# Kernel optimization log

Hardware: AMD Instinct MI355X
Metric: run time of the kernel (lower is better)

The kernel has to match this reference:

```python
import jax, jax.numpy as jnp
import numpy as np

N, IN_F, OUT_F = 8192, 512, 64
ALPHA = 0.2  # LeakyReLU negative slope


def setup_inputs() -> dict:
    key = jax.random.key(0)
    k1, k2, k3, k4 = jax.random.split(key, 4)
    x = jax.random.normal(k1, (N, IN_F), dtype=jnp.float32)
    # dense 0/1 adjacency; Bernoulli(0.5) so every row has neighbors
    adj = jax.random.randint(k2, (N, N), 0, 2, dtype=jnp.int32)
    # W stored as [in, out] (torch Linear applies x @ W.T; equivalent math)
    W = jax.random.normal(k3, (IN_F, OUT_F), dtype=jnp.float32) / np.sqrt(IN_F)
    a = jax.random.normal(k4, (2 * OUT_F,), dtype=jnp.float32) * 0.1
    return {"x": x, "adj": adj, "W": W, "a": a}


def reference(x, adj, W, a):
    # Wh: [n, out]
    Wh = x @ W
    # concat([Wh_i, Wh_j]) @ a  ==  (Wh @ a1)_i + (Wh @ a2)_j  (split 'a' in halves)
    a1, a2 = a[:OUT_F], a[OUT_F:]
    e = (Wh @ a1)[:, None] + (Wh @ a2)[None, :]          # [n, n]
    e = jnp.where(e > 0, e, ALPHA * e)                    # LeakyReLU
    e = jnp.where(adj == 0, -jnp.inf, e)                  # mask non-edges
    attn = jax.nn.softmax(e, axis=1)                      # softmax over neighbors j
    # dropout omitted: eval mode (training=False)
    return attn @ Wh                                      # [n, out]
```

## Files before the change

kernel.cpp:

```cpp
#include <hip/hip_runtime.h>
#include <cstdint>
#include <cstddef>

#define NN 8192
#define INF 512
#define OUTF 64
#define ALPHA 0.2f
#define JSPLIT 512
#define NW32 (NN / 32)
#define GEMM_BLOCKS 512
#define RSTRIDE 36

typedef _Float16 half8 __attribute__((ext_vector_type(8)));
typedef float f32x4 __attribute__((ext_vector_type(4)));

static __device__ inline unsigned short f2h(float f) {
    _Float16 h = (_Float16)f;
    return __builtin_bit_cast(unsigned short, h);
}

__global__ __launch_bounds__(256) void k01_fused(
    const float* __restrict__ x, const int* __restrict__ adj,
    const float* __restrict__ W, const float* __restrict__ a,
    unsigned short* __restrict__ Asw, float* __restrict__ U,
    unsigned short* __restrict__ e2ph, unsigned short* __restrict__ e2nh,
    unsigned* __restrict__ mask)
{
    __shared__ int ldsbuf[8192];
    const int tid = threadIdx.x;

    if (blockIdx.x >= GEMM_BLOCKS) {
        const int row = blockIdx.x - GEMM_BLOCKS;
        const int* arow = adj + (size_t)row * NN;

        #pragma unroll
        for (int k = 0; k < 8; ++k) {
            const int i = k * 1024 + tid * 4;
            int4 v = *(const int4*)(arow + i);
            const int p = i ^ (((i >> 7) & 7) << 2);
            *(int4*)&ldsbuf[p] = v;
        }
        __syncthreads();

        unsigned m = 0;
        #pragma unroll
        for (int k = 0; k < 8; ++k) {
            const int i2 = tid * 32 + k * 4;
            const int p2 = i2 ^ (((i2 >> 7) & 7) << 2);
            int4 v = *(const int4*)&ldsbuf[p2];
            m |= (v.x != 0 ? 1u : 0u) << (4 * k);
            m |= (v.y != 0 ? 1u : 0u) << (4 * k + 1);
            m |= (v.z != 0 ? 1u : 0u) << (4 * k + 2);
            m |= (v.w != 0 ? 1u : 0u) << (4 * k + 3);
        }
        mask[(size_t)row * NW32 + tid] = m;
        return;
    }

    const int i0 = blockIdx.x * 16;
    const int w  = __builtin_amdgcn_readfirstlane(tid >> 6);
    const int c  = tid & 63;
    const float* xr = x + (size_t)(i0 + 4 * w) * INF;
    const float* Wc = W + c;
    float acc[4] = {0.f, 0.f, 0.f, 0.f};

    #pragma unroll 4
    for (int kk = 0; kk < 128; ++kk) {
        const float4 x0 = *(const float4*)(xr + 0 * INF + kk * 4);
        const float4 x1 = *(const float4*)(xr + 1 * INF + kk * 4);
        const float4 x2 = *(const float4*)(xr + 2 * INF + kk * 4);
        const float4 x3 = *(const float4*)(xr + 3 * INF + kk * 4);
        const float w0 = Wc[(kk * 4 + 0) * OUTF];
        const float w1 = Wc[(kk * 4 + 1) * OUTF];
        const float w2 = Wc[(kk * 4 + 2) * OUTF];
        const float w3 = Wc[(kk * 4 + 3) * OUTF];
        acc[0] = fmaf(x0.x, w0, fmaf(x0.y, w1, fmaf(x0.z, w2, fmaf(x0.w, w3, acc[0]))));
        acc[1] = fmaf(x1.x, w0, fmaf(x1.y, w1, fmaf(x1.z, w2, fmaf(x1.w, w3, acc[1]))));
        acc[2] = fmaf(x2.x, w0, fmaf(x2.y, w1, fmaf(x2.z, w2, fmaf(x2.w, w3, acc[2]))));
        acc[3] = fmaf(x3.x, w0, fmaf(x3.y, w1, fmaf(x3.z, w2, fmaf(x3.w, w3, acc[3]))));
    }

    const float a1c = a[c];
    const float a2c = a[64 + c];
    #pragma unroll
    for (int q = 0; q < 4; ++q) {
        float v1 = acc[q] * a1c;
        float v2 = acc[q] * a2c;
        #pragma unroll
        for (int m = 32; m; m >>= 1) {
            v1 += __shfl_xor(v1, m, 64);
            v2 += __shfl_xor(v2, m, 64);
        }
        if (c == 0) {
            const int i = i0 + 4 * w + q;
            U[i]    = __expf((1.0f - ALPHA) * v1);
            e2ph[i] = f2h(__expf(v2));
            e2nh[i] = f2h(__expf(ALPHA * v2));
        }
    }

    const int i   = i0 + 4 * w;
    const int jt  = i >> 5;
    const int sub = (i >> 3) & 3;
    const int e0  = i & 7;
    ushort4 pk;
    pk.x = f2h(acc[0]); pk.y = f2h(acc[1]);
    pk.z = f2h(acc[2]); pk.w = f2h(acc[3]);
    *(ushort4*)&Asw[((size_t)(c >> 4) * 256 + jt) * 512 + ((c & 15) + 16 * sub) * 8 + e0] = pk;
}

__global__ __launch_bounds__(1024, 4) void k2_final(
    const unsigned* __restrict__ mask, const unsigned short* __restrict__ Asw,
    const float* __restrict__ Ug, const unsigned short* __restrict__ e2ph,
    const unsigned short* __restrict__ e2nh,
    float* __restrict__ out)
{
    __shared__ float red[16 * 64 * RSTRIDE];
    __shared__ float redl[16 * 32];

    const int tid   = threadIdx.x;
    const int l     = tid & 63;
    const int w     = tid >> 6;
    const int i0    = blockIdx.x * 32;
    const int jbase = w * JSPLIT;
    const int jb32  = jbase >> 5;

    const int il  = l & 15;
    const int kg  = l >> 4;
    const int kg8 = kg * 8;

    const unsigned uaw = f2h(Ug[i0 + il]);
    const unsigned ubw = f2h(Ug[i0 + 16 + il]);
    const unsigned ua2 = uaw * 0x00010001u;
    const unsigned ub2 = ubw * 0x00010001u;

    const unsigned* mbase = mask + (size_t)(i0 + il) * NW32 + jb32 + kg;
    unsigned mA[4], mB[4];
    #pragma unroll
    for (int ss = 0; ss < 4; ++ss) {
        mA[ss] = mbase[ss * 4];
        mB[ss] = mbase[(size_t)16 * NW32 + ss * 4];
    }

    f32x4 a00 = {0,0,0,0}, a01 = {0,0,0,0}, a10 = {0,0,0,0}, a11 = {0,0,0,0};
    f32x4 a20 = {0,0,0,0}, a21 = {0,0,0,0}, a30 = {0,0,0,0}, a31 = {0,0,0,0};
    f32x4 sA  = {0,0,0,0}, sB  = {0,0,0,0};

    half8 ONESH;
    #pragma unroll
    for (int e = 0; e < 8; ++e) ONESH[e] = (_Float16)1.0f;

    uint4 epc = *(const uint4*)(e2ph + jbase + kg8);
    uint4 enc = *(const uint4*)(e2nh + jbase + kg8);
    unsigned bAc = (__shfl(mA[0], il, 64) >> kg8) & 0xffu;
    unsigned bBc = (__shfl(mB[0], il, 64) >> kg8) & 0xffu;

#define SPAIR(DST, U2, EPW, ENW, BITS, R) do {                                \
    unsigned mu_, mx_;                                                        \
    asm("v_pk_mul_f16 %0, %1, %2" : "=v"(mu_) : "v"(U2), "v"(EPW));           \
    asm("v_pk_max_f16 %0, %1, %2" : "=v"(mx_) : "v"(mu_), "v"(ENW));          \
    const int lo_ = (int)((BITS) << (31 - 2 * (R))) >> 31;                    \
    const int hi_ = (int)((BITS) << (30 - 2 * (R))) >> 31;                    \
    DST = mx_ & (((unsigned)hi_ & 0xFFFF0000u) | ((unsigned)lo_ & 0x0000FFFFu)); \
} while (0)

    #pragma unroll
    for (int t = 0; t < 16; ++t) {
        const unsigned short* Ac = Asw + (size_t)(jb32 + t) * 512 + l * 8;
        half8 A0c = *(const half8*)(Ac);
        half8 A1c = *(const half8*)(Ac + 131072);
        half8 A2c = *(const half8*)(Ac + 262144);
        half8 A3c = *(const half8*)(Ac + 393216);

        const int tn = (t < 15) ? t + 1 : t;
        uint4 epn = *(const uint4*)(e2ph + jbase + tn * 32 + kg8);
        uint4 enn = *(const uint4*)(e2nh + jbase + tn * 32 + kg8);
        const int ssn = tn >> 2, ksn = tn & 3;
        unsigned bAn = (__shfl(mA[ssn], il + 16 * ksn, 64) >> kg8) & 0xffu;
        unsigned bBn = (__shfl(mB[ssn], il + 16 * ksn, 64) >> kg8) & 0xffu;

        uint4 wa, wb;
        SPAIR(wa.x, ua2, epc.x, enc.x, bAc, 0);
        SPAIR(wa.y, ua2, epc.y, enc.y, bAc, 1);
        SPAIR(wa.z, ua2, epc.z, enc.z, bAc, 2);
        SPAIR(wa.w, ua2, epc.w, enc.w, bAc, 3);
        SPAIR(wb.x, ub2, epc.x, enc.x, bBc, 0);
        SPAIR(wb.y, ub2, epc.y, enc.y, bBc, 1);
        SPAIR(wb.z, ub2, epc.z, enc.z, bBc, 2);
        SPAIR(wb.w, ub2, epc.w, enc.w, bBc, 3);
        const half8 BA = __builtin_bit_cast(half8, wa);
        const half8 BB = __builtin_bit_cast(half8, wb);

        sA = __builtin_amdgcn_mfma_f32_16x16x32_f16(ONESH, BA, sA, 0, 0, 0);
        sB = __builtin_amdgcn_mfma_f32_16x16x32_f16(ONESH, BB, sB, 0, 0, 0);

        a00 = __builtin_amdgcn_mfma_f32_16x16x32_f16(A0c, BA, a00, 0, 0, 0);
        a01 = __builtin_amdgcn_mfma_f32_16x16x32_f16(A0c, BB, a01, 0, 0, 0);
        a10 = __builtin_amdgcn_mfma_f32_16x16x32_f16(A1c, BA, a10, 0, 0, 0);
        a11 = __builtin_amdgcn_mfma_f32_16x16x32_f16(A1c, BB, a11, 0, 0, 0);
        a20 = __builtin_amdgcn_mfma_f32_16x16x32_f16(A2c, BA, a20, 0, 0, 0);
        a21 = __builtin_amdgcn_mfma_f32_16x16x32_f16(A2c, BB, a21, 0, 0, 0);
        a30 = __builtin_amdgcn_mfma_f32_16x16x32_f16(A3c, BA, a30, 0, 0, 0);
        a31 = __builtin_amdgcn_mfma_f32_16x16x32_f16(A3c, BB, a31, 0, 0, 0);

        epc = epn; enc = enn;
        bAc = bAn; bBc = bBn;
    }
#undef SPAIR

    float* rw = red + (size_t)(w * 64 + l) * RSTRIDE;
    *(float4*)(rw + 0)  = *(float4*)&a00;
    *(float4*)(rw + 4)  = *(float4*)&a01;
    *(float4*)(rw + 8)  = *(float4*)&a10;
    *(float4*)(rw + 12) = *(float4*)&a11;
    *(float4*)(rw + 16) = *(float4*)&a20;
    *(float4*)(rw + 20) = *(float4*)&a21;
    *(float4*)(rw + 24) = *(float4*)&a30;
    *(float4*)(rw + 28) = *(float4*)&a31;
    if (l < 16) {
        redl[w * 32 + il]      = sA[0];
        redl[w * 32 + 16 + il] = sB[0];
    }
    __syncthreads();

    const int row = tid >> 5;
    const int n0  = (tid & 31) * 2;
    const int h   = row >> 4;
    const int il2 = row & 15;

    float den = 0.f;
    #pragma unroll
    for (int w2 = 0; w2 < 16; ++w2) den += redl[w2 * 32 + row];
    const float inv = 1.0f / den;

    float o2[2];
    #pragma unroll
    for (int e = 0; e < 2; ++e) {
        const int n   = n0 + e;
        const int q   = n >> 4;
        const int kg2 = (n >> 2) & 3;
        const int r   = n & 3;
        float s = 0.f;
        #pragma unroll
        for (int w2 = 0; w2 < 16; ++w2)
            s += red[(size_t)(w2 * 64 + kg2 * 16 + il2) * RSTRIDE + q * 8 + h * 4 + r];
        o2[e] = s * inv;
    }
    *(float2*)&out[(size_t)(i0 + row) * OUTF + n0] = *(float2*)o2;
}

extern "C" void kernel_launch(void* const* d_in, const int* in_sizes, int n_in,
                              void* d_out, int out_size, void* d_ws, size_t ws_size,
                              hipStream_t stream) {
    const float* x   = (const float*)d_in[0];
    const int*   adj = (const int*)d_in[1];
    const float* W   = (const float*)d_in[2];
    const float* a   = (const float*)d_in[3];
    float* out = (float*)d_out;

    char* ws = (char*)d_ws;
    unsigned short* Asw = (unsigned short*)ws;
    float* U     = (float*)(ws + (1 << 20));
    unsigned short* e2ph = (unsigned short*)(ws + (1 << 20) + 32768);
    unsigned short* e2nh = (unsigned short*)(ws + (1 << 20) + 49152);
    unsigned* mask = (unsigned*)(ws + (1 << 20) + 65536);

    k01_fused<<<GEMM_BLOCKS + NN, 256, 0, stream>>>(x, adj, W, a, Asw,
                                                    U, e2ph, e2nh, mask);
    k2_final<<<NN / 32, 1024, 0, stream>>>(mask, Asw, U, e2ph, e2nh, out);
}
```

Before: 77.28 us.

## Fuse adjacency bitmask packing into attention kernel with double-buffered ballot staging

Drops the separate pass that turns the int32 adjacency matrix into a global bitmask. The attention kernel now reads adj directly, packs each 512-column slab into bits with wave ballots into double-buffered LDS, and prefetches the next slab while it runs the MFMAs on the current one. This removes the mask round trip through global memory and the extra blocks in the first kernel. In exchange the main loop gains a block-wide barrier per slab, and the 256MB adj stream now sits on the critical path of the compute kernel with only 256 blocks to hide it.

```diff
diff --git a/kernel.cpp b/kernel.cpp
--- a/kernel.cpp
+++ b/kernel.cpp
@@ -6,9 +6,6 @@
 #define INF 512
 #define OUTF 64
 #define ALPHA 0.2f
-#define JSPLIT 512
-#define NW32 (NN / 32)
-#define GEMM_BLOCKS 512
 #define RSTRIDE 36
 
 typedef _Float16 half8 __attribute__((ext_vector_type(8)));
@@ -19,47 +16,16 @@
     return __builtin_bit_cast(unsigned short, h);
 }
 
-__global__ __launch_bounds__(256) void k01_fused(
-    const float* __restrict__ x, const int* __restrict__ adj,
-    const float* __restrict__ W, const float* __restrict__ a,
-    unsigned short* __restrict__ Asw, float* __restrict__ U,
-    unsigned short* __restrict__ e2ph, unsigned short* __restrict__ e2nh,
-    unsigned* __restrict__ mask)
+__global__ __launch_bounds__(256) void k1_gemm(
+    const float* __restrict__ x, const float* __restrict__ W,
+    const float* __restrict__ a, unsigned short* __restrict__ Asw,
+    float* __restrict__ U, unsigned short* __restrict__ e2ph,
+    unsigned short* __restrict__ e2nh)
 {
-    __shared__ int ldsbuf[8192];
     const int tid = threadIdx.x;
-
-    if (blockIdx.x >= GEMM_BLOCKS) {
-        const int row = blockIdx.x - GEMM_BLOCKS;
-        const int* arow = adj + (size_t)row * NN;
-
-        #pragma unroll
-        for (int k = 0; k < 8; ++k) {
-            const int i = k * 1024 + tid * 4;
-            int4 v = *(const int4*)(arow + i);
-            const int p = i ^ (((i >> 7) & 7) << 2);
-            *(int4*)&ldsbuf[p] = v;
-        }
-        __syncthreads();
-
-        unsigned m = 0;
-        #pragma unroll
-        for (int k = 0; k < 8; ++k) {
-            const int i2 = tid * 32 + k * 4;
-            const int p2 = i2 ^ (((i2 >> 7) & 7) << 2);
-            int4 v = *(const int4*)&ldsbuf[p2];
-            m |= (v.x != 0 ? 1u : 0u) << (4 * k);
-            m |= (v.y != 0 ? 1u : 0u) << (4 * k + 1);
-            m |= (v.z != 0 ? 1u : 0u) << (4 * k + 2);
-            m |= (v.w != 0 ? 1u : 0u) << (4 * k + 3);
-        }
-        mask[(size_t)row * NW32 + tid] = m;
-        return;
-    }
-
-    const int i0 = blockIdx.x * 16;
-    const int w  = __builtin_amdgcn_readfirstlane(tid >> 6);
-    const int c  = tid & 63;
+    const int i0  = blockIdx.x * 16;
+    const int w   = __builtin_amdgcn_readfirstlane(tid >> 6);
+    const int c   = tid & 63;
     const float* xr = x + (size_t)(i0 + 4 * w) * INF;
     const float* Wc = W + c;
     float acc[4] = {0.f, 0.f, 0.f, 0.f};
@@ -109,38 +75,27 @@
     *(ushort4*)&Asw[((size_t)(c >> 4) * 256 + jt) * 512 + ((c & 15) + 16 * sub) * 8 + e0] = pk;
 }
 
-__global__ __launch_bounds__(1024, 4) void k2_final(
-    const unsigned* __restrict__ mask, const unsigned short* __restrict__ Asw,
+__global__ __launch_bounds__(1024) void k2_stream(
+    const int* __restrict__ adj, const unsigned short* __restrict__ Asw,
     const float* __restrict__ Ug, const unsigned short* __restrict__ e2ph,
     const unsigned short* __restrict__ e2nh,
     float* __restrict__ out)
 {
+    __shared__ unsigned lm[2][32][18];
     __shared__ float red[16 * 64 * RSTRIDE];
     __shared__ float redl[16 * 32];
 
-    const int tid   = threadIdx.x;
-    const int l     = tid & 63;
-    const int w     = tid >> 6;
-    const int i0    = blockIdx.x * 32;
-    const int jbase = w * JSPLIT;
-    const int jb32  = jbase >> 5;
+    const int tid = threadIdx.x;
+    const int l   = tid & 63;
+    const int w   = tid >> 6;
+    const int i0  = blockIdx.x * 32;
 
     const int il  = l & 15;
     const int kg  = l >> 4;
     const int kg8 = kg * 8;
 
-    const unsigned uaw = f2h(Ug[i0 + il]);
-    const unsigned ubw = f2h(Ug[i0 + 16 + il]);
-    const unsigned ua2 = uaw * 0x00010001u;
-    const unsigned ub2 = ubw * 0x00010001u;
-
-    const unsigned* mbase = mask + (size_t)(i0 + il) * NW32 + jb32 + kg;
-    unsigned mA[4], mB[4];
-    #pragma unroll
-    for (int ss = 0; ss < 4; ++ss) {
-        mA[ss] = mbase[ss * 4];
-        mB[ss] = mbase[(size_t)16 * NW32 + ss * 4];
-    }
+    const unsigned ua2 = (unsigned)f2h(Ug[i0 + il])      * 0x00010001u;
+    const unsigned ub2 = (unsigned)f2h(Ug[i0 + 16 + il]) * 0x00010001u;
 
     f32x4 a00 = {0,0,0,0}, a01 = {0,0,0,0}, a10 = {0,0,0,0}, a11 = {0,0,0,0};
     f32x4 a20 = {0,0,0,0}, a21 = {0,0,0,0}, a30 = {0,0,0,0}, a31 = {0,0,0,0};
@@ -150,10 +105,26 @@
     #pragma unroll
     for (int e = 0; e < 8; ++e) ONESH[e] = (_Float16)1.0f;
 
-    uint4 epc = *(const uint4*)(e2ph + jbase + kg8);
-    uint4 enc = *(const uint4*)(e2nh + jbase + kg8);
-    unsigned bAc = (__shfl(mA[0], il, 64) >> kg8) & 0xffu;
-    unsigned bBc = (__shfl(mB[0], il, 64) >> kg8) & 0xffu;
+    int vals[16];
+
+#define LOADS(SS) do {                                                        \
+    _Pragma("unroll")                                                         \
+    for (int k = 0; k < 16; ++k) {                                            \
+        const int idx = w * 16 + k;                                           \
+        vals[k] = adj[(size_t)(i0 + (idx >> 3)) * NN + (SS) * 512             \
+                      + (idx & 7) * 64 + l];                                  \
+    }                                                                         \
+} while (0)
+
+#define BALLOT_WRITE(SS) do {                                                 \
+    _Pragma("unroll")                                                         \
+    for (int k = 0; k < 16; ++k) {                                            \
+        const int idx = w * 16 + k;                                           \
+        const unsigned long long b = __ballot(vals[k] != 0);                  \
+        if (l == 0)                                                           \
+            *(unsigned long long*)&lm[(SS) & 1][idx >> 3][(idx & 7) * 2] = b; \
+    }                                                                         \
+} while (0)
 
 #define SPAIR(DST, U2, EPW, ENW, BITS, R) do {                                \
     unsigned mu_, mx_;                                                        \
@@ -164,20 +135,27 @@
     DST = mx_ & (((unsigned)hi_ & 0xFFFF0000u) | ((unsigned)lo_ & 0x0000FFFFu)); \
 } while (0)
 
-    #pragma unroll
-    for (int t = 0; t < 16; ++t) {
-        const unsigned short* Ac = Asw + (size_t)(jb32 + t) * 512 + l * 8;
+    LOADS(0);
+    BALLOT_WRITE(0);
+    __syncthreads();
+
+    for (int ss = 0; ss < 16; ++ss) {
+        if (ss < 15) LOADS(ss + 1);
+
+        const int jw = ss * 512 + w * 32;
+        const int jb = ss * 16 + w;
+
+        const unsigned short* Ac = Asw + (size_t)jb * 512 + l * 8;
         half8 A0c = *(const half8*)(Ac);
         half8 A1c = *(const half8*)(Ac + 131072);
         half8 A2c = *(const half8*)(Ac + 262144);
         half8 A3c = *(const half8*)(Ac + 393216);
 
-        const int tn = (t < 15) ? t + 1 : t;
-        uint4 epn = *(const uint4*)(e2ph + jbase + tn * 32 + kg8);
-        uint4 enn = *(const uint4*)(e2nh + jbase + tn * 32 + kg8);
-        const int ssn = tn >> 2, ksn = tn & 3;
-        unsigned bAn = (__shfl(mA[ssn], il + 16 * ksn, 64) >> kg8) & 0xffu;
-        unsigned bBn = (__shfl(mB[ssn], il + 16 * ksn, 64) >> kg8) & 0xffu;
+        uint4 epc = *(const uint4*)(e2ph + jw + kg8);
+        uint4 enc = *(const uint4*)(e2nh + jw + kg8);
+
+        const unsigned bAc = (lm[ss & 1][il][w]      >> kg8) & 0xffu;
+        const unsigned bBc = (lm[ss & 1][il + 16][w] >> kg8) & 0xffu;
 
         uint4 wa, wb;
         SPAIR(wa.x, ua2, epc.x, enc.x, bAc, 0);
@@ -203,10 +181,12 @@
         a30 = __builtin_amdgcn_mfma_f32_16x16x32_f16(A3c, BA, a30, 0, 0, 0);
         a31 = __builtin_amdgcn_mfma_f32_16x16x32_f16(A3c, BB, a31, 0, 0, 0);
 
-        epc = epn; enc = enn;
-        bAc = bAn; bBc = bBn;
+        if (ss < 15) BALLOT_WRITE(ss + 1);
+        __syncthreads();
     }
 #undef SPAIR
+#undef BALLOT_WRITE
+#undef LOADS
 
     float* rw = red + (size_t)(w * 64 + l) * RSTRIDE;
     *(float4*)(rw + 0)  = *(float4*)&a00;
@@ -263,9 +243,7 @@
     float* U     = (float*)(ws + (1 << 20));
     unsigned short* e2ph = (unsigned short*)(ws + (1 << 20) + 32768);
     unsigned short* e2nh = (unsigned short*)(ws + (1 << 20) + 49152);
-    unsigned* mask = (unsigned*)(ws + (1 << 20) + 65536);
-
-    k01_fused<<<GEMM_BLOCKS + NN, 256, 0, stream>>>(x, adj, W, a, Asw,
-                                                    U, e2ph, e2nh, mask);
-    k2_final<<<NN / 32, 1024, 0, stream>>>(mask, Asw, U, e2ph, e2nh, out);
-}
+
+    k1_gemm<<<512, 256, 0, stream>>>(x, W, a, Asw, U, e2ph, e2nh);
+    k2_stream<<<NN / 32, 1024, 0, stream>>>(adj, Asw, U, e2ph, e2nh, out);
+}
```

Measured after the change: 102.0 us. 31.9% more time.
